# Kernel tuning notes

Measured on AMD Instinct MI355X. Metric: run time of the kernel, lower is better.

## Reference

```python
import jax, jax.numpy as jnp
import numpy as np

B, C, H, W = 16, 256, 56, 56
HEADS, DHEAD = 8, 32
INNER = HEADS * DHEAD  # == C
BLOCK, HALO = 7, 3
WIN = BLOCK + 2 * HALO      # 13
REL = WIN                   # rel_size = block + 2*halo
HIDDEN = 4 * C
EPS = 1e-6
LS_INIT = 1e-6


def layernorm2d(x, w, b):
    # channels-first LayerNorm over C, x: (B,C,H,W)
    u = jnp.mean(x, axis=1, keepdims=True)
    s = jnp.mean((x - u) ** 2, axis=1, keepdims=True)
    xn = (x - u) * jax.lax.rsqrt(s + EPS)
    return w[None, :, None, None] * xn + b[None, :, None, None]


def rel_to_abs(x):
    # x: (b, l, 2r-1) -> (b, l, r)
    b, l, m = x.shape
    r = (m + 1) // 2
    x = jnp.pad(x, ((0, 0), (0, 0), (0, 1))).reshape(b, l * (m + 1))
    x = jnp.pad(x, ((0, 0), (0, m - l))).reshape(b, l + 1, m)
    return x[:, :l, -r:]


def relative_logits_1d(q, rel_k):
    # q: (b, h, w, d); rel_k: (2r-1, d) -> (b, h, r, w, r)
    b, h, w, _ = q.shape
    r = (rel_k.shape[0] + 1) // 2
    logits = jnp.einsum('bxyd,rd->bxyr', q, rel_k)
    logits = rel_to_abs(logits.reshape(b * h, w, -1)).reshape(b, h, w, r)
    return jnp.broadcast_to(logits[:, :, None], (b, h, r, w, r))


def rel_pos_bias(q, rel_h, rel_w):
    b = q.shape[0]
    r = (rel_w.shape[0] + 1) // 2
    q2 = q.reshape(b, BLOCK, BLOCK, DHEAD)
    lw = relative_logits_1d(q2, rel_w)                        # (b, x, i, y, j)
    lw = lw.transpose(0, 1, 3, 2, 4).reshape(b, BLOCK * BLOCK, r * r)
    lh = relative_logits_1d(q2.transpose(0, 2, 1, 3), rel_h)  # (b, y, i, x, j)
    lh = lh.transpose(0, 3, 1, 4, 2).reshape(b, BLOCK * BLOCK, r * r)
    return lw + lh


def halo_attention(x, wq, wkv, wo, bo, rel_h, rel_w):
    Bq, _, Hh, Ww = x.shape
    nh, nw = Hh // BLOCK, Ww // BLOCK
    nb = nh * nw
    # queries: non-overlapping blocks -> (B*nb, BLOCK^2, C)
    q_inp = x.reshape(Bq, C, nh, BLOCK, nw, BLOCK).transpose(0, 2, 4, 3, 5, 1)
    q_inp = q_inp.reshape(Bq * nb, BLOCK * BLOCK, C)
    # keys/values: overlapping haloed windows (like F.unfold with padding=HALO)
    xp = jnp.pad(x, ((0, 0), (0, 0), (HALO, HALO), (HALO, HALO)))
    rows = (jnp.arange(nh) * BLOCK)[:, None] + jnp.arange(WIN)
    cols = (jnp.arange(nw) * BLOCK)[:, None] + jnp.arange(WIN)
    kv = xp[:, :, rows][:, :, :, :, cols]
    kv = kv.transpose(0, 2, 4, 3, 5, 1).reshape(Bq * nb, WIN * WIN, C)
    q = q_inp @ wq.T
    k, v = jnp.split(kv @ wkv.T, 2, axis=-1)

    def split_heads(t):
        b2, n2, _ = t.shape
        return t.reshape(b2, n2, HEADS, DHEAD).transpose(0, 2, 1, 3).reshape(b2 * HEADS, n2, DHEAD)

    q, k, v = map(split_heads, (q, k, v))
    q = q * (DHEAD ** -0.5)
    sim = jnp.einsum('bid,bjd->bij', q, k) + rel_pos_bias(q, rel_h, rel_w)
    # mask out-of-bounds (zero-padded) halo positions
    onep = jnp.pad(jnp.ones((Hh, Ww), sim.dtype), ((HALO, HALO), (HALO, HALO)))
    m = (onep[rows][:, :, cols].transpose(0, 2, 1, 3).reshape(nb, WIN * WIN)) > 0
    sim = sim.reshape(Bq, nb, HEADS, BLOCK * BLOCK, WIN * WIN)
    sim = jnp.where(m[None, :, None, None, :], sim, -jnp.finfo(sim.dtype).max)
    sim = sim.reshape(Bq * nb * HEADS, BLOCK * BLOCK, WIN * WIN)
    attn = jax.nn.softmax(sim, axis=-1)
    out = jnp.einsum('bij,bjd->bid', attn, v)
    out = out.reshape(Bq * nb, HEADS, BLOCK * BLOCK, DHEAD).transpose(0, 2, 1, 3)
    out = out.reshape(Bq * nb, BLOCK * BLOCK, INNER) @ wo.T + bo
    out = out.reshape(Bq, nh, nw, BLOCK, BLOCK, C).transpose(0, 5, 1, 3, 2, 4)
    return out.reshape(Bq, C, Hh, Ww)


def _forward(x, ln1_w, ln1_b, ln2_w, ln2_b, wq, wkv, wo, bo, rel_h, rel_w,
             gamma1, gamma2, fc1_w, fc1_b, fc2_w, fc2_b):
    y = halo_attention(layernorm2d(x, ln1_w, ln1_b), wq, wkv, wo, bo, rel_h, rel_w)
    x = x + gamma1 * y  # drop_path = 0 -> identity
    z = layernorm2d(x, ln2_w, ln2_b).transpose(0, 2, 3, 1)  # NHWC
    z = jax.nn.gelu(z @ fc1_w.T + fc1_b, approximate=False)
    z = z @ fc2_w.T + fc2_b
    z = gamma2 * z
    return x + z.transpose(0, 3, 1, 2)


def setup_inputs() -> dict:
    key = jax.random.key(0)
    ks = jax.random.split(key, 8)
    n = lambda k, sh: jax.random.normal(k, sh, jnp.float32) * 0.02
    scale = DHEAD ** -0.5
    return dict(
        x=jax.random.normal(ks[0], (B, C, H, W), jnp.float32),
        ln1_w=jnp.ones((C,), jnp.float32), ln1_b=jnp.zeros((C,), jnp.float32),
        ln2_w=jnp.ones((C,), jnp.float32), ln2_b=jnp.zeros((C,), jnp.float32),
        wq=n(ks[1], (INNER, C)),
        wkv=n(ks[2], (2 * INNER, C)),
        wo=n(ks[3], (C, INNER)), bo=jnp.zeros((C,), jnp.float32),
        rel_h=jax.random.normal(ks[4], (2 * REL - 1, DHEAD), jnp.float32) * scale,
        rel_w=jax.random.normal(ks[5], (2 * REL - 1, DHEAD), jnp.float32) * scale,
        gamma1=jnp.full((1, C, 1, 1), LS_INIT, jnp.float32),
        gamma2=jnp.full((1, 1, 1, C), LS_INIT, jnp.float32),
        fc1_w=n(ks[6], (HIDDEN, C)), fc1_b=jnp.zeros((HIDDEN,), jnp.float32),
        fc2_w=n(ks[7], (C, HIDDEN)), fc2_b=jnp.zeros((C,), jnp.float32),
    )


def reference(x, ln1_w, ln1_b, ln2_w, ln2_b, wq, wkv, wo, bo, rel_h, rel_w,
              gamma1, gamma2, fc1_w, fc1_b, fc2_w, fc2_b):
    return _forward(x, ln1_w, ln1_b, ln2_w, ln2_b, wq, wkv, wo, bo, rel_h, rel_w,
                    gamma1, gamma2, fc1_w, fc1_b, fc2_w, fc2_b)
```

## Files before the change

kernel.cpp:

```cpp
#include <hip/hip_runtime.h>
#include <cmath>

#define DI __device__ __forceinline__

typedef unsigned short ushort_t;
typedef __attribute__((ext_vector_type(8))) short short8;
typedef __attribute__((ext_vector_type(8))) unsigned short ushort8;
typedef __attribute__((ext_vector_type(4))) unsigned short ushort4_t;
typedef __attribute__((ext_vector_type(4))) float floatx4;
typedef unsigned int u32;
typedef __attribute__((ext_vector_type(4))) u32 uintx4;

DI float bf2f(ushort_t u) {
    unsigned v = ((unsigned)u) << 16;
    float f;
    __builtin_memcpy(&f, &v, 4);
    return f;
}
DI ushort_t f2bf(float f) {
    unsigned u;
    __builtin_memcpy(&u, &f, 4);
    unsigned r = (u + 0x7FFFu + ((u >> 16) & 1u)) >> 16;
    return (ushort_t)r;
}
DI ushort_t f2bf_tr(float f) {
    unsigned u;
    __builtin_memcpy(&u, &f, 4);
    return (ushort_t)(u >> 16);
}

DI void async_copy16(const ushort_t* gsrc, ushort_t* ldst) {
    auto gp = (const __attribute__((address_space(1))) u32*)gsrc;
    auto lp = (__attribute__((address_space(3))) u32*)ldst;
    __builtin_amdgcn_global_load_lds(gp, lp, 16, 0, 0);
}


__global__ void convert_all_kernel(const float* __restrict__ wq, const float* __restrict__ wkv,
                                   const float* __restrict__ wo, const float* __restrict__ fc1w,
                                   const float* __restrict__ fc2w, const float* __restrict__ relh,
                                   const float* __restrict__ relw,
                                   ushort_t* __restrict__ bqkv, ushort_t* __restrict__ woC,
                                   ushort_t* __restrict__ fc1C, ushort_t* __restrict__ fc2C,
                                   ushort_t* __restrict__ relC, ushort_t* __restrict__ boneB) {
    int i = blockIdx.x * 256 + threadIdx.x;
    if (i < 196608) { bqkv[i] = f2bf(i < 65536 ? wq[i] : wkv[i - 65536]); return; }
    i -= 196608;
    if (i < 65536) { woC[i] = f2bf(wo[i]); return; }
    i -= 65536;
    if (i < 262144) { fc1C[i] = f2bf(fc1w[i]); return; }
    i -= 262144;
    if (i < 262144) { fc2C[i] = f2bf(fc2w[i]); return; }
    i -= 262144;
    if (i < 800) { relC[i] = f2bf(relh[i]); return; }
    i -= 800;
    if (i < 800) { relC[800 + i] = f2bf(relw[i]); return; }
    i -= 800;
    if (i < 5632) {
        int j = i >> 5, k = i & 31;
        int kh = j / 13, kw = j - kh * 13;
        ushort_t v = 0;
        if (j < 169) {
            if (k == kh || k == 13 + kw) v = 0x3F80;
            if (k == 28 && kh < 3) v = 0x3F80;
            if (k == 29 && kh >= 10) v = 0x3F80;
            if (k == 30 && kw < 3) v = 0x3F80;
            if (k == 31 && kw >= 10) v = 0x3F80;
        } else {
            if (k == 27) v = 0x3F80;
        }
        boneB[i] = v;
    }
}

__global__ __launch_bounds__(256) void ln1_kernel(const float* __restrict__ x,
                                                  const float* __restrict__ w,
                                                  const float* __restrict__ bias,
                                                  ushort_t* __restrict__ t1,
                                                  float* __restrict__ xh) {
    __shared__ __align__(16) float lds[56 * 256];
    int b = blockIdx.x / 56, h = blockIdx.x % 56;
    int c = threadIdx.x;
    const float* row = x + (((size_t)(b * 256 + c) * 56 + h) * 56);
    floatx4 vals[14];
#pragma unroll
    for (int i = 0; i < 14; i++) vals[i] = *(const floatx4*)(row + i * 4);
#pragma unroll
    for (int i = 0; i < 14; i++)
#pragma unroll
        for (int e = 0; e < 4; e++) lds[(i * 4 + e) * 256 + c] = vals[i][e];
    __syncthreads();
    int wv = threadIdx.x >> 6, lane = threadIdx.x & 63;
    for (int p0 = 0; p0 < 14; p0++) {
        int p = wv * 14 + p0;
        float xv[4];
        float s = 0.f, q = 0.f;
#pragma unroll
        for (int j = 0; j < 4; j++) {
            xv[j] = lds[p * 256 + lane * 4 + j];
            s += xv[j];
            q += xv[j] * xv[j];
        }
#pragma unroll
        for (int off = 32; off; off >>= 1) {
            s += __shfl_xor(s, off);
            q += __shfl_xor(q, off);
        }
        float mean = s * (1.f / 256.f);
        float var = q * (1.f / 256.f) - mean * mean;
        float rstd = rsqrtf(var + 1e-6f);
        size_t token = ((size_t)b * 56 + h) * 56 + p;
        ushort4_t o4;
        floatx4 x4;
#pragma unroll
        for (int j = 0; j < 4; j++) {
            int cc = lane * 4 + j;
            o4[j] = f2bf_tr(w[cc] * ((xv[j] - mean) * rstd) + bias[cc]);
            x4[j] = xv[j];
        }
        *(ushort4_t*)(t1 + token * 256 + lane * 4) = o4;
        *(floatx4*)(xh + token * 256 + lane * 4) = x4;
    }
}

template <int EPI>
__global__ __launch_bounds__(256) void gemm_kernel(const ushort_t* __restrict__ A,
                                                   const ushort_t* __restrict__ Bw,
                                                   void* __restrict__ Cout, int K, int N,
                                                   const float* __restrict__ biasf,
                                                   const float* __restrict__ resf,
                                                   const float* __restrict__ gammaf) {
    __shared__ __align__(16) ushort_t As[2][128 * 32];
    __shared__ __align__(16) ushort_t Bs[2][128 * 32];
    int m0 = blockIdx.x * 128, n0 = blockIdx.y * 128;
    int t = threadIdx.x;
    int wave = t >> 6, lane = t & 63;
    int wm = (wave & 1) * 64, wn = (wave >> 1) * 64;
    int lr = lane & 15, quad = lane >> 4;
    floatx4 acc[4][4] = {};

    int srow = t >> 2, sc16 = t & 3;
    int srow1 = srow + 64;
    const ushort_t* Arow0 = A + (size_t)(m0 + srow) * K + sc16 * 8;
    const ushort_t* Arow1 = A + (size_t)(m0 + srow1) * K + sc16 * 8;
    const ushort_t* Brow0 = Bw + (size_t)(n0 + srow) * K + sc16 * 8;
    const ushort_t* Brow1 = Bw + (size_t)(n0 + srow1) * K + sc16 * 8;

    async_copy16(Arow0, &As[0][t * 8]);
    async_copy16(Brow0, &Bs[0][t * 8]);
    async_copy16(Arow1, &As[0][(t + 256) * 8]);
    async_copy16(Brow1, &Bs[0][(t + 256) * 8]);
    __syncthreads();

    int cur = 0;
    for (int k0 = 0; k0 < K; k0 += 32) {
        if (k0 + 32 < K) {
            int nk = k0 + 32;
            async_copy16(Arow0 + nk, &As[cur ^ 1][t * 8]);
            async_copy16(Brow0 + nk, &Bs[cur ^ 1][t * 8]);
            async_copy16(Arow1 + nk, &As[cur ^ 1][(t + 256) * 8]);
            async_copy16(Brow1 + nk, &Bs[cur ^ 1][(t + 256) * 8]);
        }
        short8 af[4], bf[4];
#pragma unroll
        for (int i = 0; i < 4; i++) af[i] = *(const short8*)(&As[cur][(wm + i * 16 + lr) * 32 + quad * 8]);
#pragma unroll
        for (int i = 0; i < 4; i++) bf[i] = *(const short8*)(&Bs[cur][(wn + i * 16 + lr) * 32 + quad * 8]);
#pragma unroll
        for (int i = 0; i < 4; i++)
#pragma unroll
            for (int j = 0; j < 4; j++)
                acc[i][j] = __builtin_amdgcn_mfma_f32_16x16x32_bf16(af[i], bf[j], acc[i][j], 0, 0, 0);
        __syncthreads();
        cur ^= 1;
    }
    const float qsc = (EPI == 3 && n0 < 256) ? 0.17677669529663687f : 1.0f;
#pragma unroll
    for (int i = 0; i < 4; i++)
#pragma unroll
        for (int j = 0; j < 4; j++)
#pragma unroll
            for (int r = 0; r < 4; r++) {
                int row = m0 + wm + i * 16 + quad * 4 + r;
                int col = n0 + wn + j * 16 + lr;
                float v = acc[i][j][r];
                if (EPI == 1) {
                    v = resf[(size_t)row * N + col] + gammaf[col] * (v + biasf[col]);
                    ((float*)Cout)[(size_t)row * N + col] = v;
                } else if (EPI == 2) {
                    v += biasf[col];
                    float s = __expf(-1.702f * v);
                    v = v * __builtin_amdgcn_rcpf(1.0f + s);
                    ((ushort_t*)Cout)[(size_t)row * N + col] = f2bf_tr(v);
                } else {
                    ((ushort_t*)Cout)[(size_t)row * N + col] = f2bf_tr(v * qsc);
                }
            }
}

__global__ __launch_bounds__(256, 4) void attn_kernel(const ushort_t* __restrict__ qkv,
                                                      const ushort_t* __restrict__ relh,
                                                      const ushort_t* __restrict__ relw,
                                                      const ushort_t* __restrict__ bone,
                                                      ushort_t* __restrict__ attnout) {
    __shared__ __align__(16) char smem[30208];
    ushort_t* Vt = (ushort_t*)smem;
    ushort_t* tblA = (ushort_t*)(smem + 12800);
    ushort_t* Ks = (ushort_t*)(smem + 16896);
    ushort_t* Ps = (ushort_t*)(smem + 16896);

    int wg = blockIdx.x;
    int head = wg & 7;
    int blk = (wg >> 3) & 63;
    int b = wg >> 9;
    int bh = blk >> 3, bw = blk & 7;
    int t = threadIdx.x;
    int wave = t >> 6, lane = t & 63;
    int lr = lane & 15, quad = lane >> 4;
    const int base_tok = b * 3136;

    short8 bbr[11];
#pragma unroll
    for (int nt = 0; nt < 11; nt++)
        bbr[nt] = *(const short8*)(bone + (nt * 16 + lr) * 32 + quad * 8);
    short8 bfg4[4];
#pragma unroll
    for (int ntile = 0; ntile < 4; ntile++) {
        int n = ntile * 16 + lr;
        int eff = (n < 50) ? n : 0;
        const ushort_t* rp = (eff < 25) ? (relh + eff * 32) : (relw + (eff - 25) * 32);
        bfg4[ntile] = *(const short8*)(rp + quad * 8);
    }
    short8 aq;
    {
        int qrow = wave * 16 + lr;
        int qx = qrow / 7, qy = qrow - qx * 7;
        int tok = min(base_tok + (bh * 7 + qx) * 56 + (bw * 7 + qy), 50175);
        aq = *(const short8*)(qkv + (size_t)tok * 768 + head * 32 + quad * 8);
    }

    for (int c = t; c < 704; c += 256) {
        int j = c >> 2, ck = c & 3;
        int kh = j / 13, kw = j - kh * 13;
        int gh = bh * 7 + kh - 3, gw = bw * 7 + kw - 3;
        int tok = base_tok + gh * 56 + gw;
        tok = min(max(tok, 0), 50175);
        async_copy16(qkv + (size_t)tok * 768 + 256 + head * 32 + ck * 8, Ks + c * 8);
    }
    for (int c = t; c < 704; c += 256) {
        int ck = (c >= 528) ? 3 : (c >= 352) ? 2 : (c >= 176) ? 1 : 0;
        int j = c - ck * 176;
        int kh = j / 13, kw = j - kh * 13;
        int gh = bh * 7 + kh - 3, gw = bw * 7 + kw - 3;
        int tok = base_tok + gh * 56 + gw;
        tok = min(max(tok, 0), 50175);
        ushort8 v = *(const ushort8*)(qkv + (size_t)tok * 768 + 512 + head * 32 + ck * 8);
#pragma unroll
        for (int e = 0; e < 8; e++) Vt[(ck * 8 + e) * 200 + j] = v[e];
    }
    {
        int row = t >> 3, e2 = t & 7;
        *(u32*)(Vt + row * 200 + 176 + e2 * 2) = 0;
    }
    {
        const u32 NEG = 0xCE6Eu;
        bool himask = (t & 3) == 3;
        u32 e1 = himask ? (NEG << 16) : 0u;
        u32 e2m = himask ? ((bh == 0 ? NEG : 0u) | (bh == 7 ? NEG << 16 : 0u)) : 0u;
        u32 e3m = himask ? ((bw == 0 ? NEG : 0u) | (bw == 7 ? NEG << 16 : 0u)) : 0u;
        uintx4 ini = {0u, e1, e2m, e3m};
        *(uintx4*)(smem + 12800 + t * 16) = ini;
    }
    __syncthreads();

    floatx4 zero4 = {0.f, 0.f, 0.f, 0.f};

    int qx_r[4], qy_r[4];
#pragma unroll
    for (int r = 0; r < 4; r++) {
        int row = wave * 16 + quad * 4 + r;
        qx_r[r] = row / 7;
        qy_r[r] = row - qx_r[r] * 7;
    }

#pragma unroll
    for (int ntile = 0; ntile < 4; ntile++) {
        int n = ntile * 16 + lr;
        floatx4 cta = __builtin_amdgcn_mfma_f32_16x16x32_bf16(aq, bfg4[ntile], zero4, 0, 0, 0);
#pragma unroll
        for (int r = 0; r < 4; r++) {
            int slot = (n < 25) ? (n - 12 + qx_r[r]) : (n - 24 + qy_r[r]);
            bool ok = (n < 25) ? (slot >= 0 && slot <= 12)
                               : (n < 50 && slot >= 13 && slot <= 25);
            int ss = ok ? slot : 26;
            tblA[(wave * 16 + quad * 4 + r) * 32 + ss] = f2bf_tr(cta[r]);
        }
    }

    short8 afb = *(const short8*)(tblA + (wave * 16 + lr) * 32 + quad * 8);
    floatx4 sacc[11];
#pragma unroll
    for (int nt = 0; nt < 11; nt++) {
        short8 bk = *(const short8*)(Ks + (nt * 16 + lr) * 32 + quad * 8);
        floatx4 s0 = __builtin_amdgcn_mfma_f32_16x16x32_bf16(aq, bk, zero4, 0, 0, 0);
        sacc[nt] = __builtin_amdgcn_mfma_f32_16x16x32_bf16(afb, bbr[nt], s0, 0, 0, 0);
    }

    __syncthreads();

    float pvhi[5][4];
    float inv_[4];
#pragma unroll
    for (int r = 0; r < 4; r++) {
        int qr2 = wave * 16 + quad * 4 + r;
        float sum = 0.f;
#pragma unroll
        for (int nt = 0; nt < 11; nt++) {
            float e = __expf(sacc[nt][r]);
            sum += e;
            if (nt < 6)
                Ps[qr2 * 104 + nt * 16 + lr] = f2bf_tr(e);
            else
                pvhi[nt - 6][r] = e;
        }
#pragma unroll
        for (int off = 1; off < 16; off <<= 1) sum += __shfl_xor(sum, off);
        inv_[r] = 1.f / sum;
    }

    floatx4 oacc[2] = {zero4, zero4};
#pragma unroll
    for (int kk = 0; kk < 3; kk++) {
        int k0 = kk * 32;
        short8 ap = *(const short8*)(Ps + (wave * 16 + lr) * 104 + k0 + quad * 8);
#pragma unroll
        for (int n2 = 0; n2 < 2; n2++) {
            short8 bv = *(const short8*)(Vt + (n2 * 16 + lr) * 200 + k0 + quad * 8);
            oacc[n2] = __builtin_amdgcn_mfma_f32_16x16x32_bf16(ap, bv, oacc[n2], 0, 0, 0);
        }
    }
#pragma unroll
    for (int r = 0; r < 4; r++) {
        int qr2 = wave * 16 + quad * 4 + r;
#pragma unroll
        for (int nt = 0; nt < 5; nt++) Ps[qr2 * 104 + nt * 16 + lr] = f2bf_tr(pvhi[nt][r]);
        Ps[qr2 * 104 + 80 + lr] = 0;
    }
#pragma unroll
    for (int kk = 0; kk < 3; kk++) {
        int k0 = kk * 32;
        short8 ap = *(const short8*)(Ps + (wave * 16 + lr) * 104 + k0 + quad * 8);
#pragma unroll
        for (int n2 = 0; n2 < 2; n2++) {
            short8 bv = *(const short8*)(Vt + (n2 * 16 + lr) * 200 + 96 + k0 + quad * 8);
            oacc[n2] = __builtin_amdgcn_mfma_f32_16x16x32_bf16(ap, bv, oacc[n2], 0, 0, 0);
        }
    }

#pragma unroll
    for (int n2 = 0; n2 < 2; n2++)
#pragma unroll
        for (int r = 0; r < 4; r++) {
            int qr2 = wave * 16 + quad * 4 + r;
            if (qr2 < 49) {
                int qx = qr2 / 7, qy = qr2 - qx * 7;
                size_t tok = (size_t)base_tok + (bh * 7 + qx) * 56 + (bw * 7 + qy);
                attnout[tok * 256 + head * 32 + n2 * 16 + lr] = f2bf_tr(oacc[n2][r] * inv_[r]);
            }
        }
}

__global__ __launch_bounds__(256) void ln2_kernel(const float* __restrict__ xin,
                                                  const float* __restrict__ w,
                                                  const float* __restrict__ bias,
                                                  ushort_t* __restrict__ o) {
    int token = blockIdx.x * 4 + (threadIdx.x >> 6);
    int lane = threadIdx.x & 63;
    floatx4 v4 = *(const floatx4*)(xin + (size_t)token * 256 + lane * 4);
    float s = 0.f, q = 0.f;
#pragma unroll
    for (int i = 0; i < 4; i++) {
        s += v4[i];
        q += v4[i] * v4[i];
    }
#pragma unroll
    for (int off = 32; off; off >>= 1) {
        s += __shfl_xor(s, off);
        q += __shfl_xor(q, off);
    }
    float mean = s * (1.f / 256.f);
    float var = q * (1.f / 256.f) - mean * mean;
    float rstd = rsqrtf(var + 1e-6f);
    ushort4_t o4;
#pragma unroll
    for (int i = 0; i < 4; i++) {
        int c = lane * 4 + i;
        o4[i] = f2bf_tr(w[c] * ((v4[i] - mean) * rstd) + bias[c]);
    }
    *(ushort4_t*)(o + (size_t)token * 256 + lane * 4) = o4;
}

__global__ __launch_bounds__(256) void out_transpose_kernel(const float* __restrict__ s,
                                                            float* __restrict__ o) {
    __shared__ __align__(16) float lds[56 * 256];
    int b = blockIdx.x / 56, h = blockIdx.x % 56;
    const float* src = s + (((size_t)b * 56 + h) * 56) * 256;
    int t = threadIdx.x;
#pragma unroll
    for (int i = 0; i < 14; i++) {
        int chunk = i * 256 + t;
        *(floatx4*)(lds + chunk * 4) = *(const floatx4*)(src + chunk * 4);
    }
    __syncthreads();
    int c = t;
    float* dst = o + (((size_t)b * 256 + c) * 56 + h) * 56;
#pragma unroll
    for (int i = 0; i < 14; i++) {
        floatx4 v;
#pragma unroll
        for (int e = 0; e < 4; e++) v[e] = lds[(i * 4 + e) * 256 + c];
        *(floatx4*)(dst + i * 4) = v;
    }
}

extern "C" void kernel_launch(void* const* d_in, const int* in_sizes, int n_in,
                              void* d_out, int out_size, void* d_ws, size_t ws_size,
                              hipStream_t stream) {
    const float* x = (const float*)d_in[0];
    const float* ln1w = (const float*)d_in[1];
    const float* ln1b = (const float*)d_in[2];
    const float* ln2w = (const float*)d_in[3];
    const float* ln2b = (const float*)d_in[4];
    const float* wq = (const float*)d_in[5];
    const float* wkv = (const float*)d_in[6];
    const float* wo = (const float*)d_in[7];
    const float* bo = (const float*)d_in[8];
    const float* relh = (const float*)d_in[9];
    const float* relw = (const float*)d_in[10];
    const float* g1 = (const float*)d_in[11];
    const float* g2 = (const float*)d_in[12];
    const float* fc1w = (const float*)d_in[13];
    const float* fc1b = (const float*)d_in[14];
    const float* fc2w = (const float*)d_in[15];
    const float* fc2b = (const float*)d_in[16];
    float* out = (float*)d_out;

    char* ws = (char*)d_ws;
    float* xh = (float*)ws;
    float* x1 = xh;
    float* sbuf = xh;
    ushort_t* t1 = (ushort_t*)(ws + 51380224);
    ushort_t* attnb = t1;
    ushort_t* qkv = (ushort_t*)(ws + 77070336);
    ushort_t* t2 = qkv;
    ushort_t* hid = (ushort_t*)(ws + 77070336 + 25690112);
    ushort_t* wv_ = (ushort_t*)(ws + 154140672);
    ushort_t* bqkv = wv_;
    ushort_t* woC = wv_ + 196608;
    ushort_t* fc1C = woC + 65536;
    ushort_t* fc2C = fc1C + 262144;
    ushort_t* relC = fc2C + 262144;
    ushort_t* boneG = relC + 1600;

    convert_all_kernel<<<3101, 256, 0, stream>>>(wq, wkv, wo, fc1w, fc2w, relh, relw,
                                                 bqkv, woC, fc1C, fc2C, relC, boneG);
    ln1_kernel<<<896, 256, 0, stream>>>(x, ln1w, ln1b, t1, xh);
    gemm_kernel<3><<<dim3(392, 6), 256, 0, stream>>>(t1, bqkv, qkv, 256, 768, nullptr, nullptr, nullptr);
    attn_kernel<<<8192, 256, 0, stream>>>(qkv, relC, relC + 800, boneG, attnb);
    gemm_kernel<1><<<dim3(392, 2), 256, 0, stream>>>(attnb, woC, x1, 256, 256, bo, xh, g1);
    ln2_kernel<<<12544, 256, 0, stream>>>(x1, ln2w, ln2b, t2);
    const size_t CH = 25088;
    for (int c = 0; c < 2; c++) {
        gemm_kernel<2><<<dim3(196, 8), 256, 0, stream>>>(t2 + c * CH * 256, fc1C, hid, 256, 1024, fc1b, nullptr, nullptr);
        gemm_kernel<1><<<dim3(196, 2), 256, 0, stream>>>(hid, fc2C, sbuf + c * CH * 256, 1024, 256, fc2b, x1 + c * CH * 256, g2);
    }
    out_transpose_kernel<<<896, 256, 0, stream>>>(sbuf, out);
}
```

Before: 441.5 us.

## Permute P/V key layout for packed stores and compute softmax sum via MFMA

Reorders the key dimension of the P and V^T shared-memory tiles so each lane writes its exp values as packed 32-bit pairs instead of scattered 16-bit stores. The K async copies and V loads are merged into one unrolled loop with the V loads hoisted ahead of the transposed stores. The softmax row sum is now taken from an extra MFMA against a ones vector, replacing the cross-lane shuffle reduction, and the reciprocal uses the hardware rcp. This sums the bf16-rounded probabilities rather than the fp32 ones, and each store pass adds an extra MFMA.

Result: faster. 427.3 us (-3.2%).

```diff
diff --git a/kernel.cpp b/kernel.cpp
--- a/kernel.cpp
+++ b/kernel.cpp
@@ -27,6 +27,12 @@
     unsigned u;
     __builtin_memcpy(&u, &f, 4);
     return (ushort_t)(u >> 16);
+}
+DI u32 pack2bf(float lo, float hi) {
+    u32 a, b;
+    __builtin_memcpy(&a, &lo, 4);
+    __builtin_memcpy(&b, &hi, 4);
+    return (a >> 16) | (b & 0xFFFF0000u);
 }
 
 DI void async_copy16(const ushort_t* gsrc, ushort_t* ldst) {
@@ -239,28 +245,38 @@
         aq = *(const short8*)(qkv + (size_t)tok * 768 + head * 32 + quad * 8);
     }
 
-    for (int c = t; c < 704; c += 256) {
+    ushort8 vv[3];
+    int vrow[3], vcol[3];
+#pragma unroll
+    for (int it = 0; it < 3; it++) {
+        int c = t + it * 256;
+        bool act = (it < 2) || (t < 192);
         int j = c >> 2, ck = c & 3;
         int kh = j / 13, kw = j - kh * 13;
         int gh = bh * 7 + kh - 3, gw = bw * 7 + kw - 3;
-        int tok = base_tok + gh * 56 + gw;
-        tok = min(max(tok, 0), 50175);
-        async_copy16(qkv + (size_t)tok * 768 + 256 + head * 32 + ck * 8, Ks + c * 8);
-    }
-    for (int c = t; c < 704; c += 256) {
-        int ck = (c >= 528) ? 3 : (c >= 352) ? 2 : (c >= 176) ? 1 : 0;
-        int j = c - ck * 176;
-        int kh = j / 13, kw = j - kh * 13;
-        int gh = bh * 7 + kh - 3, gw = bw * 7 + kw - 3;
-        int tok = base_tok + gh * 56 + gw;
-        tok = min(max(tok, 0), 50175);
-        ushort8 v = *(const ushort8*)(qkv + (size_t)tok * 768 + 512 + head * 32 + ck * 8);
-#pragma unroll
-        for (int e = 0; e < 8; e++) Vt[(ck * 8 + e) * 200 + j] = v[e];
-    }
-    {
-        int row = t >> 3, e2 = t & 7;
-        *(u32*)(Vt + row * 200 + 176 + e2 * 2) = 0;
+        int tok = min(max(base_tok + gh * 56 + gw, 0), 50175);
+        const ushort_t* src = qkv + (size_t)tok * 768 + head * 32 + ck * 8;
+        if (act) {
+            async_copy16(src + 256, Ks + c * 8);
+            vv[it] = *(const ushort8*)(src + 512);
+        }
+        int nt = j >> 4, l2 = j & 15;
+        vcol[it] = (nt >= 6) ? (96 + l2 * 6 + nt - 6) : (l2 * 6 + nt);
+        vrow[it] = ck * 8;
+    }
+#pragma unroll
+    for (int it = 0; it < 3; it++) {
+        bool act = (it < 2) || (t < 192);
+        if (act) {
+#pragma unroll
+            for (int e = 0; e < 8; e++) Vt[(vrow[it] + e) * 200 + vcol[it]] = vv[it][e];
+        }
+    }
+#pragma unroll
+    for (int i = 0; i < 2; i++) {
+        int idx = t + i * 256;
+        int row = idx >> 4, l2 = idx & 15;
+        Vt[row * 200 + 96 + l2 * 6 + 5] = 0;
     }
     {
         const u32 NEG = 0xCE6Eu;
@@ -308,27 +324,28 @@
 
     __syncthreads();
 
-    float pvhi[5][4];
-    float inv_[4];
+    u32 phi[4][3];
 #pragma unroll
     for (int r = 0; r < 4; r++) {
         int qr2 = wave * 16 + quad * 4 + r;
-        float sum = 0.f;
-#pragma unroll
-        for (int nt = 0; nt < 11; nt++) {
-            float e = __expf(sacc[nt][r]);
-            sum += e;
-            if (nt < 6)
-                Ps[qr2 * 104 + nt * 16 + lr] = f2bf_tr(e);
-            else
-                pvhi[nt - 6][r] = e;
-        }
-#pragma unroll
-        for (int off = 1; off < 16; off <<= 1) sum += __shfl_xor(sum, off);
-        inv_[r] = 1.f / sum;
-    }
+        float eb[11];
+#pragma unroll
+        for (int nt = 0; nt < 11; nt++) eb[nt] = __expf(sacc[nt][r]);
+        u32* prow = (u32*)(Ps + qr2 * 104 + lr * 6);
+        prow[0] = pack2bf(eb[0], eb[1]);
+        prow[1] = pack2bf(eb[2], eb[3]);
+        prow[2] = pack2bf(eb[4], eb[5]);
+        phi[r][0] = pack2bf(eb[6], eb[7]);
+        phi[r][1] = pack2bf(eb[8], eb[9]);
+        phi[r][2] = pack2bf(eb[10], 0.f);
+    }
+
+    short8 ones8;
+#pragma unroll
+    for (int e = 0; e < 8; e++) ones8[e] = (short)0x3F80;
 
     floatx4 oacc[2] = {zero4, zero4};
+    floatx4 osum = zero4;
 #pragma unroll
     for (int kk = 0; kk < 3; kk++) {
         int k0 = kk * 32;
@@ -338,13 +355,15 @@
             short8 bv = *(const short8*)(Vt + (n2 * 16 + lr) * 200 + k0 + quad * 8);
             oacc[n2] = __builtin_amdgcn_mfma_f32_16x16x32_bf16(ap, bv, oacc[n2], 0, 0, 0);
         }
+        osum = __builtin_amdgcn_mfma_f32_16x16x32_bf16(ap, ones8, osum, 0, 0, 0);
     }
 #pragma unroll
     for (int r = 0; r < 4; r++) {
         int qr2 = wave * 16 + quad * 4 + r;
-#pragma unroll
-        for (int nt = 0; nt < 5; nt++) Ps[qr2 * 104 + nt * 16 + lr] = f2bf_tr(pvhi[nt][r]);
-        Ps[qr2 * 104 + 80 + lr] = 0;
+        u32* prow = (u32*)(Ps + qr2 * 104 + lr * 6);
+        prow[0] = phi[r][0];
+        prow[1] = phi[r][1];
+        prow[2] = phi[r][2];
     }
 #pragma unroll
     for (int kk = 0; kk < 3; kk++) {
@@ -355,6 +374,7 @@
             short8 bv = *(const short8*)(Vt + (n2 * 16 + lr) * 200 + 96 + k0 + quad * 8);
             oacc[n2] = __builtin_amdgcn_mfma_f32_16x16x32_bf16(ap, bv, oacc[n2], 0, 0, 0);
         }
+        osum = __builtin_amdgcn_mfma_f32_16x16x32_bf16(ap, ones8, osum, 0, 0, 0);
     }
 
 #pragma unroll
@@ -363,9 +383,10 @@
         for (int r = 0; r < 4; r++) {
             int qr2 = wave * 16 + quad * 4 + r;
             if (qr2 < 49) {
+                float inv = __builtin_amdgcn_rcpf(osum[r]);
                 int qx = qr2 / 7, qy = qr2 - qx * 7;
                 size_t tok = (size_t)base_tok + (bh * 7 + qx) * 56 + (bw * 7 + qy);
-                attnout[tok * 256 + head * 32 + n2 * 16 + lr] = f2bf_tr(oacc[n2][r] * inv_[r]);
+                attnout[tok * 256 + head * 32 + n2 * 16 + lr] = f2bf_tr(oacc[n2][r] * inv);
             }
         }
 }
```
